# Optimization experiments

Measured on AMD Instinct MI355X. Metric: run time of the kernel, lower is better.

The kernel has to match this reference:

```python
import jax, jax.numpy as jnp
import numpy as np

N_NODES = 100000
N_EDGES = 1600000
IN_CH = 128
HEADS = 4
OUT_CH = 32
NEG_SLOPE = 0.2
EPS = 1e-10


def setup_inputs() -> dict:
    key = jax.random.key(0)
    k1, k2, k3, k4 = jax.random.split(key, 4)
    x = jax.random.normal(k1, (N_NODES, IN_CH), dtype=jnp.float32)
    edge_index = jax.random.randint(k2, (2, N_EDGES), 0, N_NODES, dtype=jnp.int64)
    # small scale keeps exp(-leakyrelu(score)) numerically tame
    W = jax.random.normal(k3, (IN_CH, HEADS * OUT_CH), dtype=jnp.float32) * 0.05
    attention = jax.random.normal(k4, (HEADS, 2 * OUT_CH), dtype=jnp.float32) * 0.05
    bias = jnp.zeros((HEADS * OUT_CH,), dtype=jnp.float32)
    return {"x": x, "edge_index": edge_index, "W": W, "attention": attention, "bias": bias}


def reference(x, edge_index, W, attention, bias):
    N = x.shape[0]
    H, two_o = attention.shape
    O = two_o // 2
    # shared fc_src == fc_tgt (in_channels is an int in the original)
    h = (x @ W).reshape(N, H, O)  # [N, H, O]
    # attention vector splits over the concat [h_src || h_tgt]
    a_src, a_tgt = attention[:, :O], attention[:, O:]
    s_src = jnp.einsum('nho,ho->nh', h, a_src)  # [N, H]
    s_tgt = jnp.einsum('nho,ho->nh', h, a_tgt)  # [N, H]
    src, tgt = edge_index[0], edge_index[1]
    score = s_src[src] + s_tgt[tgt]  # [E, H]
    # NOTE: original applies exp to the NEGATED LeakyReLU output
    e = jnp.exp(-jax.nn.leaky_relu(score, NEG_SLOPE))  # [E, H]
    # numerator: sum_j e_ij * h_src[j] scattered to target nodes
    num = jax.ops.segment_sum(e[:, :, None] * h[src], tgt, num_segments=N)  # [N, H, O]
    den = jax.ops.segment_sum(e, tgt, num_segments=N)  # [N, H]
    out = num / jnp.clip(den, EPS, None)[:, :, None]
    out = out.reshape(N, H * O)  # concat=True
    return out + bias
```

## Files before the change

kernel.cpp:

```cpp
#include <hip/hip_runtime.h>
#include <stdint.h>


#define NN 100000
#define EE 1600000
#define INCH 128
#define HO 128
#define HEADS 4
#define OUTC 32

#define BSH 8
#define NBUCK ((NN + 255) >> BSH)
#define CAPBK 5120
#define CHA 4096
#define ABLK ((EE + CHA - 1) / CHA)

typedef unsigned short ushort_t;
typedef unsigned int uint_t;
typedef __attribute__((ext_vector_type(8))) short bf16x8;
typedef __attribute__((ext_vector_type(4))) float f32x4;

__device__ __forceinline__ float bfl(uint_t u) { return __uint_as_float(u << 16); }
__device__ __forceinline__ float bfh(uint_t u) { return __uint_as_float(u & 0xffff0000u); }
__device__ __forceinline__ uint_t f2bf(float f) {
    uint_t u = __float_as_uint(f);
    u = (u + 0x7fffu + ((u >> 16) & 1u)) >> 16;
    return u;
}
__device__ __forceinline__ float att_w(float sc) {
    return __expf(-(sc > 0.f ? sc : 0.2f * sc));
}

__global__ __launch_bounds__(256) void prepW_k(const float* __restrict__ W,
                                               ushort_t* __restrict__ gWtHi,
                                               ushort_t* __restrict__ gWtLo) {
    const int gidx = blockIdx.x * 256 + threadIdx.x;
    const int col = gidx & 127;
    const int k = gidx >> 7;
    const float v = W[k * 128 + col];
    const uint_t h = f2bf(v);
    const uint_t lo = f2bf(v - bfl(h));
    gWtHi[col * 128 + k] = (ushort_t)h;
    gWtLo[col * 128 + k] = (ushort_t)lo;
}

__global__ __launch_bounds__(256) void gemm_h(const float* __restrict__ x,
                                              const ushort_t* __restrict__ gWtHi,
                                              const ushort_t* __restrict__ gWtLo,
                                              const float* __restrict__ att,
                                              ushort_t* __restrict__ hb,
                                              float* __restrict__ s_src,
                                              float* __restrict__ s_tgt) {
    __shared__ __align__(16) char smem[16384];
    ushort_t* xHi  = (ushort_t*)smem;
    ushort_t* xLo  = (ushort_t*)(smem + 8192);
    const int tid = threadIdx.x;
    const int row0 = blockIdx.x * 32;

    const int lane = tid & 63;
    const int w = tid >> 6;
    const int l15 = lane & 15;
    const int g = lane >> 4;
    const int swz = (l15 & 7) << 4;

    bf16x8 bh[2][4], bl[2][4];
    {
        const ushort_t* pH = gWtHi + (size_t)(w * 32 + l15) * 128 + g * 8;
        const ushort_t* pL = gWtLo + (size_t)(w * 32 + l15) * 128 + g * 8;
#pragma unroll
        for (int ntl = 0; ntl < 2; ++ntl)
#pragma unroll
            for (int ks = 0; ks < 4; ++ks) {
                bh[ntl][ks] = *(const bf16x8*)(pH + ntl * 16 * 128 + ks * 32);
                bl[ntl][ks] = *(const bf16x8*)(pL + ntl * 16 * 128 + ks * 32);
            }
    }

    {
        const float4* x4 = (const float4*)(x + (size_t)row0 * INCH);
#pragma unroll
        for (int j = 0; j < 4; ++j) {
            const int i = tid + 256 * j;
            const int row = i >> 5;
            const int k4 = i & 31;
            const float4 v = x4[i];
            const uint_t h0 = f2bf(v.x), h1 = f2bf(v.y), h2 = f2bf(v.z), h3 = f2bf(v.w);
            const uint_t l0 = f2bf(v.x - bfl(h0));
            const uint_t l1 = f2bf(v.y - bfl(h1));
            const uint_t l2 = f2bf(v.z - bfl(h2));
            const uint_t l3 = f2bf(v.w - bfl(h3));
            const int byteOff = (row * 256 + k4 * 8) ^ ((row & 7) << 4);
            *(uint2*)((char*)xHi + byteOff) = make_uint2(h0 | (h1 << 16), h2 | (h3 << 16));
            *(uint2*)((char*)xLo + byteOff) = make_uint2(l0 | (l1 << 16), l2 | (l3 << 16));
        }
    }
    __syncthreads();

    f32x4 acc[2][2] = {};
#pragma unroll
    for (int ks = 0; ks < 4; ++ks) {
        const int kb = ks * 64 + g * 16;
        const bf16x8 a0h = *(const bf16x8*)((char*)xHi + ((l15 * 256 + kb) ^ swz));
        const bf16x8 a1h = *(const bf16x8*)((char*)xHi + (((16 + l15) * 256 + kb) ^ swz));
        const bf16x8 a0l = *(const bf16x8*)((char*)xLo + ((l15 * 256 + kb) ^ swz));
        const bf16x8 a1l = *(const bf16x8*)((char*)xLo + (((16 + l15) * 256 + kb) ^ swz));
        acc[0][0] = __builtin_amdgcn_mfma_f32_16x16x32_bf16(a0h, bh[0][ks], acc[0][0], 0, 0, 0);
        acc[0][1] = __builtin_amdgcn_mfma_f32_16x16x32_bf16(a0h, bh[1][ks], acc[0][1], 0, 0, 0);
        acc[1][0] = __builtin_amdgcn_mfma_f32_16x16x32_bf16(a1h, bh[0][ks], acc[1][0], 0, 0, 0);
        acc[1][1] = __builtin_amdgcn_mfma_f32_16x16x32_bf16(a1h, bh[1][ks], acc[1][1], 0, 0, 0);
        acc[0][0] = __builtin_amdgcn_mfma_f32_16x16x32_bf16(a0h, bl[0][ks], acc[0][0], 0, 0, 0);
        acc[0][1] = __builtin_amdgcn_mfma_f32_16x16x32_bf16(a0h, bl[1][ks], acc[0][1], 0, 0, 0);
        acc[1][0] = __builtin_amdgcn_mfma_f32_16x16x32_bf16(a1h, bl[0][ks], acc[1][0], 0, 0, 0);
        acc[1][1] = __builtin_amdgcn_mfma_f32_16x16x32_bf16(a1h, bl[1][ks], acc[1][1], 0, 0, 0);
        acc[0][0] = __builtin_amdgcn_mfma_f32_16x16x32_bf16(a0l, bh[0][ks], acc[0][0], 0, 0, 0);
        acc[0][1] = __builtin_amdgcn_mfma_f32_16x16x32_bf16(a0l, bh[1][ks], acc[0][1], 0, 0, 0);
        acc[1][0] = __builtin_amdgcn_mfma_f32_16x16x32_bf16(a1l, bh[0][ks], acc[1][0], 0, 0, 0);
        acc[1][1] = __builtin_amdgcn_mfma_f32_16x16x32_bf16(a1l, bh[1][ks], acc[1][1], 0, 0, 0);
    }

#pragma unroll
    for (int mt = 0; mt < 2; ++mt)
#pragma unroll
        for (int ntl = 0; ntl < 2; ++ntl) {
            const int col = w * 32 + ntl * 16 + l15;
#pragma unroll
            for (int r = 0; r < 4; ++r) {
                const int row = row0 + mt * 16 + g * 4 + r;
                hb[(size_t)row * HO + col] = (ushort_t)f2bf(acc[mt][ntl][r]);
            }
        }

    const float cs0 = att[w * 64 + l15];
    const float cs1 = att[w * 64 + 16 + l15];
    const float ct0 = att[w * 64 + 32 + l15];
    const float ct1 = att[w * 64 + 48 + l15];
#pragma unroll
    for (int mt = 0; mt < 2; ++mt)
#pragma unroll
        for (int r = 0; r < 4; ++r) {
            float ps = acc[mt][0][r] * cs0 + acc[mt][1][r] * cs1;
            float pt = acc[mt][0][r] * ct0 + acc[mt][1][r] * ct1;
#pragma unroll
            for (int d = 1; d < 16; d <<= 1) {
                ps += __shfl_xor(ps, d, 64);
                pt += __shfl_xor(pt, d, 64);
            }
            if (l15 == 0) {
                const int row = row0 + mt * 16 + g * 4 + r;
                s_src[row * 4 + w] = ps;
                s_tgt[row * 4 + w] = pt;
            }
        }
}

__global__ __launch_bounds__(512) void bucketA_k(const int* __restrict__ ei,
                                                 int* __restrict__ gcur,
                                                 uint_t* __restrict__ grec) {
    __shared__ int hist[NBUCK];
    __shared__ int gbase[NBUCK];
    __shared__ int lcur[NBUCK];
    const int tid = threadIdx.x;
    const int e0 = blockIdx.x * CHA;
    const int cnt = min(CHA, EE - e0);

    for (int b = tid; b < NBUCK; b += 512) hist[b] = 0;
    __syncthreads();
    for (int i = tid; i < cnt; i += 512)
        atomicAdd(&hist[ei[EE + e0 + i] >> BSH], 1);
    __syncthreads();
    for (int b = tid; b < NBUCK; b += 512) {
        const int h = hist[b];
        gbase[b] = b * CAPBK + (h ? atomicAdd(&gcur[b], h) : 0);
        lcur[b] = 0;
    }
    __syncthreads();
    for (int i = tid; i < cnt; i += 512) {
        const int src = ei[e0 + i];
        const int tgt = ei[EE + e0 + i];
        const int b = tgt >> BSH;
        const int p = atomicAdd(&lcur[b], 1);
        grec[gbase[b] + p] = (uint_t)src | ((uint_t)(tgt & 255) << 17);
    }
}

__global__ __launch_bounds__(1024) void bucketB_k(const int* __restrict__ bucketCnt,
                                                  const uint_t* __restrict__ grec,
                                                  const float* __restrict__ s_src,
                                                  const float* __restrict__ s_tgt,
                                                  int2* __restrict__ offs2,
                                                  int* __restrict__ sorted_src,
                                                  float4* __restrict__ wgt) {
    __shared__ int cur[256];
    __shared__ int scn[256];
    __shared__ uint_t sbuf[CAPBK];
    const int tid = threadIdx.x;
    const int b = blockIdx.x;
    const int n0 = b << BSH;
    const int nn = min(256, NN - n0);
    const int R0 = b * CAPBK;
    const int cnt = min(bucketCnt[b], CAPBK);

    if (tid < 256) cur[tid] = 0;
    __syncthreads();
    uint_t r0v = 0xFFFFFFFFu, r1v = 0xFFFFFFFFu, r2v = 0xFFFFFFFFu,
           r3v = 0xFFFFFFFFu, r4v = 0xFFFFFFFFu;
    {
        int i = tid;
        if (i < cnt) { r0v = grec[R0 + i]; atomicAdd(&cur[r0v >> 17], 1); } i += 1024;
        if (i < cnt) { r1v = grec[R0 + i]; atomicAdd(&cur[r1v >> 17], 1); } i += 1024;
        if (i < cnt) { r2v = grec[R0 + i]; atomicAdd(&cur[r2v >> 17], 1); } i += 1024;
        if (i < cnt) { r3v = grec[R0 + i]; atomicAdd(&cur[r3v >> 17], 1); } i += 1024;
        if (i < cnt) { r4v = grec[R0 + i]; atomicAdd(&cur[r4v >> 17], 1); }
    }
    __syncthreads();
    int v = 0;
    if (tid < 256) { v = cur[tid]; scn[tid] = v; }
    __syncthreads();
#pragma unroll
    for (int off = 1; off < 256; off <<= 1) {
        int u = (tid < 256 && tid >= off) ? scn[tid - off] : 0;
        __syncthreads();
        if (tid < 256) scn[tid] += u;
        __syncthreads();
    }
    if (tid < 256) {
        const int ex = scn[tid] - v;
        cur[tid] = ex;
        if (tid < nn) offs2[n0 + tid] = make_int2(R0 + ex, R0 + ex + v);
    }
    __syncthreads();
    if (r0v != 0xFFFFFFFFu) sbuf[atomicAdd(&cur[r0v >> 17], 1)] = r0v;
    if (r1v != 0xFFFFFFFFu) sbuf[atomicAdd(&cur[r1v >> 17], 1)] = r1v;
    if (r2v != 0xFFFFFFFFu) sbuf[atomicAdd(&cur[r2v >> 17], 1)] = r2v;
    if (r3v != 0xFFFFFFFFu) sbuf[atomicAdd(&cur[r3v >> 17], 1)] = r3v;
    if (r4v != 0xFFFFFFFFu) sbuf[atomicAdd(&cur[r4v >> 17], 1)] = r4v;
    __syncthreads();
    for (int i = tid; i < cnt; i += 1024) {
        const uint_t r = sbuf[i];
        const int src = (int)(r & 0x1FFFF);
        const int tl = (int)(r >> 17);
        sorted_src[R0 + i] = src;
        const float4 ss = *(const float4*)(s_src + src * 4);
        const float4 st = *(const float4*)(s_tgt + (n0 + tl) * 4);
        float4 wv;
        wv.x = att_w(ss.x + st.x);
        wv.y = att_w(ss.y + st.y);
        wv.z = att_w(ss.z + st.z);
        wv.w = att_w(ss.w + st.w);
        wgt[R0 + i] = wv;
    }
}

__device__ __forceinline__ void gstep(int pe, int hd, int c0,
                                      const int* __restrict__ sorted_src,
                                      const float4* __restrict__ wgt,
                                      const ushort_t* __restrict__ hb,
                                      float ax[8], float& wsum) {
    const int s = sorted_src[pe];
    const float4 wq = wgt[pe];
    const float w = (hd & 2) ? ((hd & 1) ? wq.w : wq.z)
                             : ((hd & 1) ? wq.y : wq.x);
    const uint4 v = *(const uint4*)(hb + (size_t)s * HO + c0);
    ax[0] = fmaf(w, bfl(v.x), ax[0]); ax[1] = fmaf(w, bfh(v.x), ax[1]);
    ax[2] = fmaf(w, bfl(v.y), ax[2]); ax[3] = fmaf(w, bfh(v.y), ax[3]);
    ax[4] = fmaf(w, bfl(v.z), ax[4]); ax[5] = fmaf(w, bfh(v.z), ax[5]);
    ax[6] = fmaf(w, bfl(v.w), ax[6]); ax[7] = fmaf(w, bfh(v.w), ax[7]);
    wsum += w;
}

__global__ __launch_bounds__(256) void gather_k(const int2* __restrict__ offs2,
                                                const int* __restrict__ sorted_src,
                                                const float* __restrict__ wgt,
                                                const ushort_t* __restrict__ hb,
                                                const float* __restrict__ bias,
                                                float* __restrict__ out) {
    const int n = blockIdx.x * 4 + (threadIdx.x >> 6);
    const int l = threadIdx.x & 63;
    const int eg = l >> 4;
    const int ch16 = l & 15;
    const int hd = ch16 >> 2;
    const int c0 = ch16 * 8;
    const int2 pr = offs2[n];
    const int pend = pr.y;
    const float4* wgt4 = (const float4*)wgt;
    float ax[8] = {};
    float wsum = 0.f;
    for (int p = pr.x; p < pend; p += 32) {
#pragma unroll
        for (int j = 0; j < 8; ++j) {
            const int pe = p + j * 4 + eg;
            if (pe < pend)
                gstep(pe, hd, c0, sorted_src, wgt4, hb, ax, wsum);
        }
    }
#pragma unroll
    for (int d = 16; d <= 32; d <<= 1) {
#pragma unroll
        for (int j = 0; j < 8; ++j) ax[j] += __shfl_xor(ax[j], d, 64);
        wsum += __shfl_xor(wsum, d, 64);
    }
    if (eg == 0) {
        const float inv = 1.f / fmaxf(wsum, 1e-10f);
        const float4 b0 = *(const float4*)(bias + c0);
        const float4 b1 = *(const float4*)(bias + c0 + 4);
        float4 o0, o1;
        o0.x = fmaf(ax[0], inv, b0.x); o0.y = fmaf(ax[1], inv, b0.y);
        o0.z = fmaf(ax[2], inv, b0.z); o0.w = fmaf(ax[3], inv, b0.w);
        o1.x = fmaf(ax[4], inv, b1.x); o1.y = fmaf(ax[5], inv, b1.y);
        o1.z = fmaf(ax[6], inv, b1.z); o1.w = fmaf(ax[7], inv, b1.w);
        *(float4*)(out + (size_t)n * HO + c0) = o0;
        *(float4*)(out + (size_t)n * HO + c0 + 4) = o1;
    }
}

extern "C" void kernel_launch(void* const* d_in, const int* in_sizes, int n_in,
                              void* d_out, int out_size, void* d_ws, size_t ws_size,
                              hipStream_t stream) {
    const float* x    = (const float*)d_in[0];
    const int*   ei   = (const int*)d_in[1];
    const float* W    = (const float*)d_in[2];
    const float* att  = (const float*)d_in[3];
    const float* bias = (const float*)d_in[4];
    float* out = (float*)d_out;

    char* ws = (char*)d_ws;
    const size_t HB_B  = (size_t)NN * HO * 2;
    const size_t SS_B  = (size_t)NBUCK * CAPBK * 4;
    const size_t GR_B  = (size_t)NBUCK * CAPBK * 4;
    const size_t WG_B  = (size_t)NBUCK * CAPBK * 16;
    const size_t S_B   = (size_t)NN * HEADS * 4;
    const size_t OF_B  = ((size_t)NN * 8 + 15) & ~15ull;
    const size_t GC_B  = ((size_t)NBUCK * 4 + 15) & ~15ull;
    const size_t WT_B  = 32768;

    size_t o = 0;
    ushort_t* hb         = (ushort_t*)(ws + o); o += HB_B;
    int*      sorted_src = (int*)(ws + o); o += SS_B;
    uint_t*   grec       = (uint_t*)(ws + o); o += GR_B;
    float4*   wgt        = (float4*)(ws + o); o += WG_B;
    float*    ssrc       = (float*)(ws + o); o += S_B;
    float*    stgt       = (float*)(ws + o); o += S_B;
    int2*     offs2      = (int2*)(ws + o); o += OF_B;
    int*      gcur       = (int*)(ws + o); o += GC_B;
    ushort_t* gWtHi      = (ushort_t*)(ws + o); o += WT_B;
    ushort_t* gWtLo      = (ushort_t*)(ws + o); o += WT_B;

    (void)hipMemsetAsync(gcur, 0, GC_B, stream);

    prepW_k<<<64, 256, 0, stream>>>(W, gWtHi, gWtLo);
    gemm_h<<<NN / 32, 256, 0, stream>>>(x, gWtHi, gWtLo, att,
                                        hb, ssrc, stgt);
    bucketA_k<<<ABLK, 512, 0, stream>>>(ei, gcur, grec);
    bucketB_k<<<NBUCK, 1024, 0, stream>>>(gcur, grec, ssrc, stgt,
                                          offs2, sorted_src, wgt);
    gather_k<<<NN / 4, 256, 0, stream>>>(offs2, sorted_src, (const float*)wgt,
                                         hb, bias, out);
}
```

Baseline: 268.0 us.

## Restructure gather so each wave processes one edge at a time across all channels

The gather kernel now assigns each lane two channels of the 128-wide row instead of splitting lanes into four edge groups with eight channels each. Source indices are loaded cooperatively once per 64 edges and broadcast with readlane, and eight edges are batched per step to expose memory-level parallelism. This removes the cross-lane shuffle reduction at the end and the per-edge float4 weight loads, but each lane now issues narrower 4-byte gathers and more loop iterations per edge.

```diff
diff --git a/kernel.cpp b/kernel.cpp
--- a/kernel.cpp
+++ b/kernel.cpp
@@ -251,21 +251,31 @@
     }
 }
 
-__device__ __forceinline__ void gstep(int pe, int hd, int c0,
-                                      const int* __restrict__ sorted_src,
-                                      const float4* __restrict__ wgt,
-                                      const ushort_t* __restrict__ hb,
-                                      float ax[8], float& wsum) {
-    const int s = sorted_src[pe];
-    const float4 wq = wgt[pe];
-    const float w = (hd & 2) ? ((hd & 1) ? wq.w : wq.z)
-                             : ((hd & 1) ? wq.y : wq.x);
-    const uint4 v = *(const uint4*)(hb + (size_t)s * HO + c0);
-    ax[0] = fmaf(w, bfl(v.x), ax[0]); ax[1] = fmaf(w, bfh(v.x), ax[1]);
-    ax[2] = fmaf(w, bfl(v.y), ax[2]); ax[3] = fmaf(w, bfh(v.y), ax[3]);
-    ax[4] = fmaf(w, bfl(v.z), ax[4]); ax[5] = fmaf(w, bfh(v.z), ax[5]);
-    ax[6] = fmaf(w, bfl(v.w), ax[6]); ax[7] = fmaf(w, bfh(v.w), ax[7]);
-    wsum += w;
+template <bool PRED>
+__device__ __forceinline__ void gat8(const float* __restrict__ wgt,
+                                     const ushort_t* __restrict__ hb,
+                                     int srcv, int p0, int p1, int base, int e, int m,
+                                     int hd, int c0, float& ax, float& ay, float& wsum) {
+    int s[8]; float w[8]; uint_t v[8];
+#pragma unroll
+    for (int j = 0; j < 8; ++j)
+        s[j] = __builtin_amdgcn_readlane(srcv, (e + j) & 63);
+#pragma unroll
+    for (int j = 0; j < 8; ++j) {
+        int idx = p0 + base + e + j;
+        if (PRED) idx = min(idx, p1 - 1);
+        const float wl = wgt[(uint_t)idx * 4u + hd];
+        w[j] = (PRED && (e + j >= m)) ? 0.f : wl;
+    }
+#pragma unroll
+    for (int j = 0; j < 8; ++j)
+        v[j] = *(const uint_t*)(hb + (uint_t)(s[j] * HO + c0));
+#pragma unroll
+    for (int j = 0; j < 8; ++j) {
+        ax = fmaf(w[j], bfl(v[j]), ax);
+        ay = fmaf(w[j], bfh(v[j]), ay);
+    }
+    wsum += ((w[0] + w[1]) + (w[2] + w[3])) + ((w[4] + w[5]) + (w[6] + w[7]));
 }
 
 __global__ __launch_bounds__(256) void gather_k(const int2* __restrict__ offs2,
@@ -276,41 +286,26 @@
                                                 float* __restrict__ out) {
     const int n = blockIdx.x * 4 + (threadIdx.x >> 6);
     const int l = threadIdx.x & 63;
-    const int eg = l >> 4;
-    const int ch16 = l & 15;
-    const int hd = ch16 >> 2;
-    const int c0 = ch16 * 8;
+    const int c0 = l * 2;
+    const int hd = l >> 4;
     const int2 pr = offs2[n];
-    const int pend = pr.y;
-    const float4* wgt4 = (const float4*)wgt;
-    float ax[8] = {};
-    float wsum = 0.f;
-    for (int p = pr.x; p < pend; p += 32) {
-#pragma unroll
-        for (int j = 0; j < 8; ++j) {
-            const int pe = p + j * 4 + eg;
-            if (pe < pend)
-                gstep(pe, hd, c0, sorted_src, wgt4, hb, ax, wsum);
-        }
-    }
-#pragma unroll
-    for (int d = 16; d <= 32; d <<= 1) {
-#pragma unroll
-        for (int j = 0; j < 8; ++j) ax[j] += __shfl_xor(ax[j], d, 64);
-        wsum += __shfl_xor(wsum, d, 64);
-    }
-    if (eg == 0) {
-        const float inv = 1.f / fmaxf(wsum, 1e-10f);
-        const float4 b0 = *(const float4*)(bias + c0);
-        const float4 b1 = *(const float4*)(bias + c0 + 4);
-        float4 o0, o1;
-        o0.x = fmaf(ax[0], inv, b0.x); o0.y = fmaf(ax[1], inv, b0.y);
-        o0.z = fmaf(ax[2], inv, b0.z); o0.w = fmaf(ax[3], inv, b0.w);
-        o1.x = fmaf(ax[4], inv, b1.x); o1.y = fmaf(ax[5], inv, b1.y);
-        o1.z = fmaf(ax[6], inv, b1.z); o1.w = fmaf(ax[7], inv, b1.w);
-        *(float4*)(out + (size_t)n * HO + c0) = o0;
-        *(float4*)(out + (size_t)n * HO + c0 + 4) = o1;
-    }
+    const int p0 = pr.x, p1 = pr.y;
+    const int deg = p1 - p0;
+    float ax = 0.f, ay = 0.f, wsum = 0.f;
+    for (int base = 0; base < deg; base += 64) {
+        const int m = min(deg - base, 64);
+        const int srcv = sorted_src[p0 + base + ((l < m) ? l : 0)];
+        int e = 0;
+        for (; e + 8 <= m; e += 8)
+            gat8<false>(wgt, hb, srcv, p0, p1, base, e, m, hd, c0, ax, ay, wsum);
+        if (e < m)
+            gat8<true>(wgt, hb, srcv, p0, p1, base, e, m, hd, c0, ax, ay, wsum);
+    }
+    const float inv = 1.f / fmaxf(wsum, 1e-10f);
+    float2 o;
+    o.x = ax * inv + bias[c0];
+    o.y = ay * inv + bias[c0 + 1];
+    *(float2*)(out + (size_t)n * HO + c0) = o;
 }
 
 extern "C" void kernel_launch(void* const* d_in, const int* in_sizes, int n_in,
```

After: 243.6 us. 1.1x faster.
